# Kernel optimization log

Hardware: AMD Instinct MI355X
Metric: run time of the kernel (lower is better)

## Reference

```python
import jax, jax.numpy as jnp
import numpy as np
import math

B, N = 1, 768
C1, C2 = 384, 128
H, SQK, SV, PQK, PV, NC = 12, 16, 16, 4, 8, 384
EPS = 1e-8
SCALAR_W = math.sqrt(1.0 / (3.0 * SQK))           # sqrt(1/(num_logit_terms*scalar_variance))
POINT_W = math.sqrt(1.0 / (3.0 * (PQK * 9.0 / 2.0)))
W2D = math.sqrt(1.0 / 3.0)


def _quat_to_rot(q):
    # q: [..., 4] -> orthonormal rotation matrices [..., 3, 3]
    q = q / jnp.linalg.norm(q, axis=-1, keepdims=True)
    w, x, y, z = q[..., 0], q[..., 1], q[..., 2], q[..., 3]
    r0 = jnp.stack([1 - 2 * (y * y + z * z), 2 * (x * y - w * z), 2 * (x * z + w * y)], -1)
    r1 = jnp.stack([2 * (x * y + w * z), 1 - 2 * (x * x + z * z), 2 * (y * z - w * x)], -1)
    r2 = jnp.stack([2 * (x * z - w * y), 2 * (y * z + w * x), 1 - 2 * (x * x + y * y)], -1)
    return jnp.stack([r0, r1, r2], -2)


def setup_inputs() -> dict:
    key = jax.random.key(0)
    ks = jax.random.split(key, 12)

    def lin(k, o, i):
        kw, kb = jax.random.split(k)
        w = jax.random.normal(kw, (o, i), jnp.float32) / np.sqrt(i).astype(np.float32)
        b = jax.random.normal(kb, (o,), jnp.float32) * 0.01
        return w, b

    w_qs, b_qs = lin(ks[0], H * SQK, C1)
    w_kvs, b_kvs = lin(ks[1], H * (SV + SQK), C1)
    w_qp, b_qp = lin(ks[2], H * 3 * PQK, C1)
    w_kvp, b_kvp = lin(ks[3], H * 3 * (PQK + PV), C1)
    w_a2, b_a2 = lin(ks[4], H, C2)
    w_o, b_o = lin(ks[5], NC, H * (C2 + SV + 4 * PV))
    return {
        'inputs_1d': jax.random.normal(ks[6], (B, N, C1), jnp.float32),
        'inputs_2d': jax.random.normal(ks[7], (B, N, N, C2), jnp.float32),
        'mask': jnp.ones((B, N, 1), jnp.float32),
        'rotation': _quat_to_rot(jax.random.normal(ks[8], (B, N, 4), jnp.float32)),
        'translation': jax.random.normal(ks[9], (B, N, 3), jnp.float32) * 10.0,
        'w_q_scalar': w_qs, 'b_q_scalar': b_qs,
        'w_kv_scalar': w_kvs, 'b_kv_scalar': b_kvs,
        'w_q_point': w_qp, 'b_q_point': b_qp,
        'w_kv_point': w_kvp, 'b_kv_point': b_kvp,
        'tpw': jnp.ones((H,), jnp.float32),
        'w_attn2d': w_a2, 'b_attn2d': b_a2,
        'w_out': w_o, 'b_out': b_o,
    }


def ipa_forward(inputs_1d, inputs_2d, mask, rotation, translation,
                w_q_scalar, b_q_scalar, w_kv_scalar, b_kv_scalar,
                w_q_point, b_q_point, w_kv_point, b_kv_point,
                tpw, w_attn2d, b_attn2d, w_out, b_out):
    Bs, Ns, _ = inputs_1d.shape

    # scalar q/k/v
    q_scalar = (inputs_1d @ w_q_scalar.T + b_q_scalar).reshape(Bs, Ns, H, SQK)
    kv_scalar = (inputs_1d @ w_kv_scalar.T + b_kv_scalar).reshape(Bs, Ns, H, SQK + SV)
    k_scalar, v_scalar = kv_scalar[..., :SQK], kv_scalar[..., SQK:]

    # point q/k/v in local frame; split order is 3 coord chunks of size H*P
    qp = (inputs_1d @ w_q_point.T + b_q_point).reshape(Bs, Ns, 3, H * PQK)
    kvp = (inputs_1d @ w_kv_point.T + b_kv_point).reshape(Bs, Ns, 3, H * (PQK + PV))
    # to global frame: p_global = R @ p_local + t
    qg = jnp.einsum('bnij,bnjm->bnim', rotation, qp) + translation[..., None]
    kvg = jnp.einsum('bnij,bnjm->bnim', rotation, kvp) + translation[..., None]
    q_point = qg.reshape(Bs, Ns, 3, H, PQK).transpose(0, 3, 1, 4, 2)          # [B,H,N,Pqk,3]
    kv_point = kvg.reshape(Bs, Ns, 3, H, PQK + PV).transpose(0, 3, 1, 4, 2)    # [B,H,N,Pqk+Pv,3]
    k_point, v_point = kv_point[..., :PQK, :], kv_point[..., PQK:, :]

    # point-distance attention term: sum_{p,c} (q-k)^2 = |q|^2 + |k|^2 - 2 q.k
    pw = jax.nn.softplus(tpw) * POINT_W                                       # [H]
    qn = jnp.sum(q_point * q_point, axis=(-1, -2))                             # [B,H,N]
    kn = jnp.sum(k_point * k_point, axis=(-1, -2))
    qk = jnp.einsum('bhipc,bhjpc->bhij', q_point, k_point)
    dist2 = qn[..., :, None] + kn[..., None, :] - 2.0 * qk                     # [B,H,N,N]
    attn_qk_point = -0.5 * pw[None, :, None, None] * dist2

    # scalar attention term
    attn_qk_scalar = jnp.einsum('bihd,bjhd->bhij', SCALAR_W * q_scalar, k_scalar)

    # pair-bias term
    a2d = inputs_2d @ w_attn2d.T + b_attn2d                                    # [B,N,N,H]
    logits = attn_qk_scalar + attn_qk_point + W2D * a2d.transpose(0, 3, 1, 2)

    mask2d = mask * jnp.swapaxes(mask, -1, -2)                                 # [B,N,N]
    logits = logits - 1e5 * (1.0 - mask2d[:, None, :, :])
    attn = jax.nn.softmax(logits, axis=-1)                                     # [B,H,N,N]

    # scalar values
    result_scalar = jnp.einsum('bhij,bjhd->bihd', attn, v_scalar).reshape(Bs, Ns, H * SV)

    # point values (global), then back to local frame: p_local = R^T (p - t)
    rpg = jnp.einsum('bhij,bhjpc->bhipc', attn, v_point)                       # [B,H,N,Pv,3]
    rpg = rpg.transpose(0, 2, 4, 1, 3).reshape(Bs, Ns, 3, H * PV)              # [B,N,3,M]
    local = jnp.einsum('bnji,bnjm->bnim', rotation, rpg - translation[..., None])
    dist = jnp.sqrt(EPS + jnp.sum(local * local, axis=2))                      # [B,N,M]

    # attention over pair features
    r2d = jnp.einsum('bhij,bijc->bihc', attn, inputs_2d).reshape(Bs, Ns, H * C2)

    final_act = jnp.concatenate(
        [result_scalar, local[:, :, 0], local[:, :, 1], local[:, :, 2], dist, r2d], axis=-1)
    return final_act @ w_out.T + b_out


def reference(inputs_1d, inputs_2d, mask, rotation, translation,
              w_q_scalar, b_q_scalar, w_kv_scalar, b_kv_scalar,
              w_q_point, b_q_point, w_kv_point, b_kv_point,
              tpw, w_attn2d, b_attn2d, w_out, b_out):
    return ipa_forward(inputs_1d, inputs_2d, mask, rotation, translation,
                       w_q_scalar, b_q_scalar, w_kv_scalar, b_kv_scalar,
                       w_q_point, b_q_point, w_kv_point, b_kv_point,
                       tpw, w_attn2d, b_attn2d, w_out, b_out)
```

## Files before the change

### kernel.cpp

```cpp
#include <hip/hip_runtime.h>
#include <hip/hip_bf16.h>
#include <math.h>

#define NRES 768
#define C1 384
#define C2 128
#define NH 12
#define HB 6

#define OFF_QS   0
#define OFF_KS   147456
#define OFF_VS   294912
#define OFF_QPT  442368
#define OFF_KPT  552960
#define OFF_VPT  663552
#define OFF_FA   884736
#define OFF_RAW  OFF_FA

__device__ __forceinline__ float dot4(float4 a, float4 b) {
    return fmaf(a.x, b.x, fmaf(a.y, b.y, fmaf(a.z, b.z, a.w * b.w)));
}

static constexpr float SCALAR_W = 0.14433756729740643f;
static constexpr float POINT_W  = 0.13608276348795434f;
static constexpr float W2D_W    = 0.57735026918962576f;

__device__ __forceinline__ void wsel(int o,
    const float* w_qs, const float* b_qs, const float* w_kvs, const float* b_kvs,
    const float* w_qp, const float* b_qp, const float* w_kvp, const float* b_kvp,
    const float** row, float* bias)
{
    if (o < 192)      { *row = w_qs  + (size_t)o * C1;         *bias = b_qs[o]; }
    else if (o < 576) { *row = w_kvs + (size_t)(o - 192) * C1; *bias = b_kvs[o - 192]; }
    else if (o < 720) { *row = w_qp  + (size_t)(o - 576) * C1; *bias = b_qp[o - 576]; }
    else              { *row = w_kvp + (size_t)(o - 720) * C1; *bias = b_kvp[o - 720]; }
}

__global__ __launch_bounds__(256) void k1_gemm(
    const float* __restrict__ in1d,
    const float* __restrict__ w_qs, const float* __restrict__ b_qs,
    const float* __restrict__ w_kvs, const float* __restrict__ b_kvs,
    const float* __restrict__ w_qp, const float* __restrict__ b_qp,
    const float* __restrict__ w_kvp, const float* __restrict__ b_kvp,
    float* __restrict__ ws)
{
    __shared__ __align__(16) float ASt[32][68];
    __shared__ __align__(16) float WSt[32][68];
    const int t = threadIdx.x;
    const int n0 = blockIdx.x * 64;
    const int o0 = blockIdx.y * 64;
    const int tx = t & 15, ty = t >> 4;
    float acc[4][4];
    #pragma unroll
    for (int r = 0; r < 4; ++r)
        #pragma unroll
        for (int c = 0; c < 4; ++c) acc[r][c] = 0.f;

    for (int k0 = 0; k0 < C1; k0 += 32) {
        __syncthreads();
        #pragma unroll
        for (int s = 0; s < 2; ++s) {
            int q = t + 256 * s;
            int row = q >> 3, kq = (q & 7) * 4;
            float4 a4 = *(const float4*)&in1d[(size_t)(n0 + row) * C1 + k0 + kq];
            ASt[kq + 0][row] = a4.x; ASt[kq + 1][row] = a4.y;
            ASt[kq + 2][row] = a4.z; ASt[kq + 3][row] = a4.w;
            const float* wr; float bb;
            wsel(o0 + row, w_qs, b_qs, w_kvs, b_kvs, w_qp, b_qp, w_kvp, b_kvp, &wr, &bb);
            float4 w4 = *(const float4*)&wr[k0 + kq];
            WSt[kq + 0][row] = w4.x; WSt[kq + 1][row] = w4.y;
            WSt[kq + 2][row] = w4.z; WSt[kq + 3][row] = w4.w;
        }
        __syncthreads();
        #pragma unroll
        for (int k = 0; k < 32; ++k) {
            float4 a4 = *(const float4*)&ASt[k][ty * 4];
            float4 w4 = *(const float4*)&WSt[k][tx * 4];
            float av[4] = {a4.x, a4.y, a4.z, a4.w};
            float wv[4] = {w4.x, w4.y, w4.z, w4.w};
            #pragma unroll
            for (int r = 0; r < 4; ++r)
                #pragma unroll
                for (int c = 0; c < 4; ++c)
                    acc[r][c] = fmaf(av[r], wv[c], acc[r][c]);
        }
    }
    float bias[4];
    #pragma unroll
    for (int c = 0; c < 4; ++c) {
        const float* dummy;
        wsel(o0 + tx * 4 + c, w_qs, b_qs, w_kvs, b_kvs, w_qp, b_qp, w_kvp, b_kvp, &dummy, &bias[c]);
    }
    float* raw = ws + OFF_RAW;
    #pragma unroll
    for (int r = 0; r < 4; ++r) {
        int n = n0 + ty * 4 + r;
        *(float4*)&raw[(size_t)n * 1152 + o0 + tx * 4] =
            make_float4(acc[r][0] + bias[0], acc[r][1] + bias[1],
                        acc[r][2] + bias[2], acc[r][3] + bias[3]);
    }
}

__global__ __launch_bounds__(256) void k1b_scatter(
    const float* __restrict__ rot, const float* __restrict__ trans,
    float* __restrict__ ws)
{
    __shared__ __align__(16) float rawS[1152];
    const int t = threadIdx.x;
    const int i = blockIdx.x;
    const float* raw = ws + OFF_RAW + (size_t)i * 1152;
    for (int q = t; q < 288; q += 256) *(float4*)&rawS[q * 4] = *(const float4*)&raw[q * 4];
    __syncthreads();
    float* qs  = ws + OFF_QS;  float* ks  = ws + OFF_KS;  float* vs  = ws + OFF_VS;
    float* qpt = ws + OFF_QPT; float* kpt = ws + OFF_KPT; float* vpt = ws + OFF_VPT;

    for (int o = t; o < 576; o += 256) {
        float v = rawS[o];
        if (o < 192) {
            qs[(size_t)i * 192 + o] = v * SCALAR_W;
        } else {
            int idx = o - 192, h = idx >> 5, d = idx & 31;
            if (d < 16) ks[(size_t)i * 192 + h * 16 + d] = v;
            else        vs[(size_t)i * 192 + h * 16 + (d - 16)] = v;
        }
    }
    if (t < 192) {
        int m = t;
        float x0, x1, x2;
        if (m < 48) { x0 = rawS[576 + m]; x1 = rawS[624 + m]; x2 = rawS[672 + m]; }
        else { int mm = m - 48; x0 = rawS[720 + mm]; x1 = rawS[864 + mm]; x2 = rawS[1008 + mm]; }
        float g[3];
        #pragma unroll
        for (int ii = 0; ii < 3; ++ii)
            g[ii] = rot[i * 9 + ii * 3 + 0] * x0 + rot[i * 9 + ii * 3 + 1] * x1 +
                    rot[i * 9 + ii * 3 + 2] * x2 + trans[i * 3 + ii];
        if (m < 48) {
            #pragma unroll
            for (int ii = 0; ii < 3; ++ii) qpt[(size_t)i * 144 + 3 * m + ii] = g[ii];
        } else {
            int mm = m - 48, h = mm / 12, pp = mm % 12;
            if (pp < 4) {
                #pragma unroll
                for (int ii = 0; ii < 3; ++ii) kpt[(size_t)i * 144 + h * 12 + pp * 3 + ii] = g[ii];
            } else {
                #pragma unroll
                for (int ii = 0; ii < 3; ++ii) vpt[(size_t)i * 288 + h * 24 + (pp - 4) * 3 + ii] = g[ii];
            }
        }
    }
}

__global__ __launch_bounds__(256, 6) void k2_attn(
    const float* __restrict__ in2d,
    const float* __restrict__ mask,
    const float* __restrict__ rot, const float* __restrict__ trans,
    const float* __restrict__ tpw,
    const float* __restrict__ w2d, const float* __restrict__ b2d,
    float* __restrict__ ws)
{
    __shared__ __align__(16) float P[HB][264];
    __shared__ __align__(16) float qsS[192];
    __shared__ __align__(16) float qptS[144];
    __shared__ float qnS[HB], phS[HB], bbS[HB], mS[HB], lS[HB], aS[HB];
    __shared__ float rpgS[144];
    const int t  = threadIdx.x;
    const int hg = blockIdx.x;
    const int i  = blockIdx.y;
    const int h0 = hg * HB;

    const float* qs  = ws + OFF_QS;  const float* ks  = ws + OFF_KS;  const float* vs = ws + OFF_VS;
    const float* qpt = ws + OFF_QPT; const float* kpt = ws + OFF_KPT; const float* vpt = ws + OFF_VPT;

    if (t < 48) *(float4*)&qsS[t * 4] = *(const float4*)&qs[(size_t)i * 192 + t * 4];
    else if (t >= 64 && t < 100) { int u = t - 64; *(float4*)&qptS[u * 4] = *(const float4*)&qpt[(size_t)i * 144 + u * 4]; }
    __syncthreads();
    if (t < HB) {
        int h = h0 + t;
        float s = 0.f;
        #pragma unroll
        for (int e = 0; e < 12; ++e) { float x = qptS[h * 12 + e]; s += x * x; }
        qnS[t] = s;
        phS[t] = -0.5f * POINT_W * logf(1.f + __expf(tpw[h]));
        bbS[t] = W2D_W * b2d[h];
        mS[t] = -1e30f;
        lS[t] = 0.f;
    }
    __syncthreads();
    const float mi = mask[i];

    float ra[4] = {0.f, 0.f, 0.f, 0.f};
    float rb[4] = {0.f, 0.f, 0.f, 0.f};
    const bool isR2 = (t < 192);
    int lh = 0, c4 = 0, o0 = 0, q0 = 0, vh = 0;
    const float* vbase = nullptr; int vstride = 0; bool vact = false;
    if (isR2) { lh = t >> 5; c4 = t & 31; }
    else {
        int u = t - 192; vact = (u < 30); o0 = u * 8;
        if (vact) {
            if (u < 12) { vh = u >> 1; vbase = vs + (size_t)h0 * 16 + o0; vstride = 192; }
            else { q0 = o0 - 96; vh = q0 / 24; vbase = vpt + (size_t)h0 * 24 + q0; vstride = 288; }
        }
    }

    for (int tile = 0; tile < 3; ++tile) {
        const int j0 = tile * 256;
        __syncthreads();
        {
            const int j = j0 + t;
            float acc[HB];
            #pragma unroll
            for (int g = 0; g < HB; ++g) acc[g] = 0.f;
            const float* row   = in2d + ((size_t)i * NRES + j) * C2;
            const float* wbase = w2d + (size_t)h0 * C2;
            #pragma unroll 8
            for (int cc = 0; cc < 32; ++cc) {
                float4 v4 = *(const float4*)&row[cc * 4];
                #pragma unroll
                for (int g = 0; g < HB; ++g) {
                    float4 w4 = *(const float4*)&wbase[g * C2 + cc * 4];
                    acc[g] += dot4(v4, w4);
                }
            }
            const float msub = -100000.0f * (1.0f - mi * mask[j]);
            const float* ksr  = ks  + (size_t)j * 192 + h0 * 16;
            const float* kptr = kpt + (size_t)j * 144 + h0 * 12;
            #pragma unroll
            for (int g = 0; g < HB; ++g) {
                float sq = 0.f;
                #pragma unroll
                for (int d4 = 0; d4 < 4; ++d4) {
                    float4 q4 = *(const float4*)&qsS[(h0 + g) * 16 + d4 * 4];
                    float4 k4 = *(const float4*)&ksr[g * 16 + d4 * 4];
                    sq += dot4(q4, k4);
                }
                float qk = 0.f, kk = 0.f;
                #pragma unroll
                for (int e4 = 0; e4 < 3; ++e4) {
                    float4 qp4 = *(const float4*)&qptS[(h0 + g) * 12 + e4 * 4];
                    float4 kp4 = *(const float4*)&kptr[g * 12 + e4 * 4];
                    qk += dot4(qp4, kp4);
                    kk += dot4(kp4, kp4);
                }
                P[g][t] = sq + phS[g] * (qnS[g] + kk - 2.f * qk) + W2D_W * acc[g] + bbS[g] + msub;
            }
        }
        __syncthreads();
        {
            int wv = t >> 6, lane = t & 63;
            for (int g = wv; g < HB; g += 4) {
                float v0 = P[g][lane], v1 = P[g][lane + 64], v2 = P[g][lane + 128], v3 = P[g][lane + 192];
                float mt = fmaxf(fmaxf(v0, v1), fmaxf(v2, v3));
                #pragma unroll
                for (int off = 32; off > 0; off >>= 1) mt = fmaxf(mt, __shfl_xor(mt, off));
                float mold = mS[g];
                float mnew = fmaxf(mold, mt);
                float e0 = __expf(v0 - mnew), e1 = __expf(v1 - mnew);
                float e2 = __expf(v2 - mnew), e3 = __expf(v3 - mnew);
                P[g][lane] = e0; P[g][lane + 64] = e1; P[g][lane + 128] = e2; P[g][lane + 192] = e3;
                float s = e0 + e1 + e2 + e3;
                #pragma unroll
                for (int off = 32; off > 0; off >>= 1) s += __shfl_xor(s, off);
                if (lane == 0) {
                    float a = __expf(mold - mnew);
                    aS[g] = a;
                    lS[g] = lS[g] * a + s;
                    mS[g] = mnew;
                }
            }
        }
        __syncthreads();
        if (isR2) {
            float a = aS[lh];
            #pragma unroll
            for (int k = 0; k < 4; ++k) ra[k] *= a;
            const float* r2base = in2d + ((size_t)i * NRES + j0) * C2 + c4 * 4;
            for (int jj = 0; jj < 256; jj += 4) {
                float4 p4 = *(const float4*)&P[lh][jj];
                float w[4] = {p4.x, p4.y, p4.z, p4.w};
                #pragma unroll
                for (int k = 0; k < 4; ++k) {
                    float4 v4 = *(const float4*)&r2base[(size_t)(jj + k) * C2];
                    ra[0] = fmaf(w[k], v4.x, ra[0]); ra[1] = fmaf(w[k], v4.y, ra[1]);
                    ra[2] = fmaf(w[k], v4.z, ra[2]); ra[3] = fmaf(w[k], v4.w, ra[3]);
                }
            }
        } else if (vact) {
            float a = aS[vh];
            #pragma unroll
            for (int k = 0; k < 4; ++k) { ra[k] *= a; rb[k] *= a; }
            for (int jj = 0; jj < 256; jj += 4) {
                const int jg = j0 + jj;
                float4 p = *(const float4*)&P[vh][jj];
                float w[4] = {p.x, p.y, p.z, p.w};
                #pragma unroll
                for (int k = 0; k < 4; ++k) {
                    float4 va4 = *(const float4*)&vbase[(size_t)(jg + k) * vstride];
                    float4 vb4 = *(const float4*)&vbase[(size_t)(jg + k) * vstride + 4];
                    ra[0] = fmaf(w[k], va4.x, ra[0]); ra[1] = fmaf(w[k], va4.y, ra[1]);
                    ra[2] = fmaf(w[k], va4.z, ra[2]); ra[3] = fmaf(w[k], va4.w, ra[3]);
                    rb[0] = fmaf(w[k], vb4.x, rb[0]); rb[1] = fmaf(w[k], vb4.y, rb[1]);
                    rb[2] = fmaf(w[k], vb4.z, rb[2]); rb[3] = fmaf(w[k], vb4.w, rb[3]);
                }
            }
        }
    }
    float* fa = ws + OFF_FA + (size_t)i * 2112;
    if (isR2) {
        float nv = 1.f / lS[lh];
        *(float4*)&fa[576 + (h0 + lh) * 128 + c4 * 4] = make_float4(ra[0] * nv, ra[1] * nv, ra[2] * nv, ra[3] * nv);
    } else if (vact) {
        float nv = 1.f / lS[vh];
        if (o0 < 96) {
            *(float4*)&fa[h0 * 16 + o0]     = make_float4(ra[0] * nv, ra[1] * nv, ra[2] * nv, ra[3] * nv);
            *(float4*)&fa[h0 * 16 + o0 + 4] = make_float4(rb[0] * nv, rb[1] * nv, rb[2] * nv, rb[3] * nv);
        } else {
            *(float4*)&rpgS[q0]     = make_float4(ra[0] * nv, ra[1] * nv, ra[2] * nv, ra[3] * nv);
            *(float4*)&rpgS[q0 + 4] = make_float4(rb[0] * nv, rb[1] * nv, rb[2] * nv, rb[3] * nv);
        }
    }
    __syncthreads();
    if (t < 48) {
        int g = t >> 3, p = t & 7;
        int gh = h0 + g;
        float rv[3];
        #pragma unroll
        for (int c = 0; c < 3; ++c) rv[c] = rpgS[g * 24 + p * 3 + c] - trans[i * 3 + c];
        float l0 = rot[i * 9 + 0] * rv[0] + rot[i * 9 + 3] * rv[1] + rot[i * 9 + 6] * rv[2];
        float l1 = rot[i * 9 + 1] * rv[0] + rot[i * 9 + 4] * rv[1] + rot[i * 9 + 7] * rv[2];
        float l2 = rot[i * 9 + 2] * rv[0] + rot[i * 9 + 5] * rv[1] + rot[i * 9 + 8] * rv[2];
        float dd = sqrtf(1e-8f + l0 * l0 + l1 * l1 + l2 * l2);
        fa[192 + gh * 8 + p] = l0;
        fa[288 + gh * 8 + p] = l1;
        fa[384 + gh * 8 + p] = l2;
        fa[480 + gh * 8 + p] = dd;
    }
}

__global__ __launch_bounds__(256) void k3_out(
    const float* __restrict__ w_out, const float* __restrict__ b_out,
    const float* __restrict__ ws, float* __restrict__ out)
{
    __shared__ __align__(16) float ASt[32][34];
    __shared__ __align__(16) float WSt[32][34];
    const int t = threadIdx.x;
    const int i0 = blockIdx.x * 32;
    const int o0 = blockIdx.y * 32;
    const float* fa = ws + OFF_FA;
    int tx = t & 15, ty = t >> 4;
    float acc00 = 0.f, acc01 = 0.f, acc10 = 0.f, acc11 = 0.f;
    int r = t >> 3, kq = (t & 7) * 4;

    for (int k0 = 0; k0 < 2112; k0 += 32) {
        __syncthreads();
        {
            float4 a4 = *(const float4*)&fa[(size_t)(i0 + r) * 2112 + k0 + kq];
            ASt[kq + 0][r] = a4.x; ASt[kq + 1][r] = a4.y; ASt[kq + 2][r] = a4.z; ASt[kq + 3][r] = a4.w;
            float4 w4 = *(const float4*)&w_out[(size_t)(o0 + r) * 2112 + k0 + kq];
            WSt[kq + 0][r] = w4.x; WSt[kq + 1][r] = w4.y; WSt[kq + 2][r] = w4.z; WSt[kq + 3][r] = w4.w;
        }
        __syncthreads();
        #pragma unroll
        for (int k = 0; k < 32; ++k) {
            float2 av = *(const float2*)&ASt[k][ty * 2];
            float2 wv = *(const float2*)&WSt[k][tx * 2];
            acc00 = fmaf(av.x, wv.x, acc00);
            acc01 = fmaf(av.x, wv.y, acc01);
            acc10 = fmaf(av.y, wv.x, acc10);
            acc11 = fmaf(av.y, wv.y, acc11);
        }
    }
    int oi = i0 + ty * 2, oo = o0 + tx * 2;
    out[(size_t)oi * 384 + oo]           = acc00 + b_out[oo];
    out[(size_t)oi * 384 + oo + 1]       = acc01 + b_out[oo + 1];
    out[(size_t)(oi + 1) * 384 + oo]     = acc10 + b_out[oo];
    out[(size_t)(oi + 1) * 384 + oo + 1] = acc11 + b_out[oo + 1];
}

extern "C" void kernel_launch(void* const* d_in, const int* in_sizes, int n_in,
                              void* d_out, int out_size, void* d_ws, size_t ws_size,
                              hipStream_t stream) {
    const float* in1d  = (const float*)d_in[0];
    const float* in2d  = (const float*)d_in[1];
    const float* mask  = (const float*)d_in[2];
    const float* rot   = (const float*)d_in[3];
    const float* trans = (const float*)d_in[4];
    const float* w_qs  = (const float*)d_in[5];
    const float* b_qs  = (const float*)d_in[6];
    const float* w_kvs = (const float*)d_in[7];
    const float* b_kvs = (const float*)d_in[8];
    const float* w_qp  = (const float*)d_in[9];
    const float* b_qp  = (const float*)d_in[10];
    const float* w_kvp = (const float*)d_in[11];
    const float* b_kvp = (const float*)d_in[12];
    const float* tpw   = (const float*)d_in[13];
    const float* w2d   = (const float*)d_in[14];
    const float* b2d   = (const float*)d_in[15];
    const float* w_out = (const float*)d_in[16];
    const float* b_out = (const float*)d_in[17];
    float* ws  = (float*)d_ws;
    float* out = (float*)d_out;

    hipLaunchKernelGGL(k1_gemm, dim3(12, 18), dim3(256), 0, stream,
                       in1d, w_qs, b_qs, w_kvs, b_kvs, w_qp, b_qp, w_kvp, b_kvp, ws);
    hipLaunchKernelGGL(k1b_scatter, dim3(768), dim3(256), 0, stream,
                       rot, trans, ws);
    hipLaunchKernelGGL(k2_attn, dim3(2, 768), dim3(256), 0, stream,
                       in2d, mask, rot, trans, tpw, w2d, b2d, ws);
    hipLaunchKernelGGL(k3_out, dim3(24, 12), dim3(256), 0, stream,
                       w_out, b_out, ws, out);
}
```

Measured before the change: 871.1 us.

## Stage pair-feature tiles in shared memory and reorder attention grid

The pair-feature weighted sum now loads 32-row tiles of inputs_2d into shared memory cooperatively with all 256 threads, then the R2 threads read from LDS instead of doing strided global loads directly. The grid is also transposed so that consecutive blocks cover different residues i for the same head group. The tiling adds 16 syncthreads per chunk and 16 KB of LDS, which may lower occupancy under launch_bounds(256,6). It also still reads in2d once per head group.

New measurement: 882.4 us. Within noise of the previous version (+1.3%).

```diff
diff --git a/kernel.cpp b/kernel.cpp
--- a/kernel.cpp
+++ b/kernel.cpp
@@ -158,14 +158,15 @@
     const float* __restrict__ w2d, const float* __restrict__ b2d,
     float* __restrict__ ws)
 {
+    __shared__ __align__(16) float tileS[32][128];
     __shared__ __align__(16) float P[HB][264];
     __shared__ __align__(16) float qsS[192];
     __shared__ __align__(16) float qptS[144];
     __shared__ float qnS[HB], phS[HB], bbS[HB], mS[HB], lS[HB], aS[HB];
     __shared__ float rpgS[144];
     const int t  = threadIdx.x;
-    const int hg = blockIdx.x;
-    const int i  = blockIdx.y;
+    const int i  = blockIdx.x;
+    const int hg = blockIdx.y;
     const int h0 = hg * HB;
 
     const float* qs  = ws + OFF_QS;  const float* ks  = ws + OFF_KS;  const float* vs = ws + OFF_VS;
@@ -273,33 +274,48 @@
             float a = aS[lh];
             #pragma unroll
             for (int k = 0; k < 4; ++k) ra[k] *= a;
-            const float* r2base = in2d + ((size_t)i * NRES + j0) * C2 + c4 * 4;
-            for (int jj = 0; jj < 256; jj += 4) {
-                float4 p4 = *(const float4*)&P[lh][jj];
-                float w[4] = {p4.x, p4.y, p4.z, p4.w};
-                #pragma unroll
-                for (int k = 0; k < 4; ++k) {
-                    float4 v4 = *(const float4*)&r2base[(size_t)(jj + k) * C2];
-                    ra[0] = fmaf(w[k], v4.x, ra[0]); ra[1] = fmaf(w[k], v4.y, ra[1]);
-                    ra[2] = fmaf(w[k], v4.z, ra[2]); ra[3] = fmaf(w[k], v4.w, ra[3]);
-                }
-            }
         } else if (vact) {
             float a = aS[vh];
             #pragma unroll
             for (int k = 0; k < 4; ++k) { ra[k] *= a; rb[k] *= a; }
-            for (int jj = 0; jj < 256; jj += 4) {
-                const int jg = j0 + jj;
-                float4 p = *(const float4*)&P[vh][jj];
-                float w[4] = {p.x, p.y, p.z, p.w};
-                #pragma unroll
-                for (int k = 0; k < 4; ++k) {
-                    float4 va4 = *(const float4*)&vbase[(size_t)(jg + k) * vstride];
-                    float4 vb4 = *(const float4*)&vbase[(size_t)(jg + k) * vstride + 4];
-                    ra[0] = fmaf(w[k], va4.x, ra[0]); ra[1] = fmaf(w[k], va4.y, ra[1]);
-                    ra[2] = fmaf(w[k], va4.z, ra[2]); ra[3] = fmaf(w[k], va4.w, ra[3]);
-                    rb[0] = fmaf(w[k], vb4.x, rb[0]); rb[1] = fmaf(w[k], vb4.y, rb[1]);
-                    rb[2] = fmaf(w[k], vb4.z, rb[2]); rb[3] = fmaf(w[k], vb4.w, rb[3]);
+        }
+        for (int sub = 0; sub < 8; ++sub) {
+            __syncthreads();
+            #pragma unroll
+            for (int u2 = 0; u2 < 4; ++u2) {
+                int q = u2 * 256 + t;
+                int rr = q >> 5, cc = q & 31;
+                *(float4*)&tileS[rr][cc * 4] =
+                    *(const float4*)&in2d[((size_t)i * NRES + j0 + sub * 32 + rr) * C2 + cc * 4];
+            }
+            __syncthreads();
+            if (isR2) {
+                for (int jj = 0; jj < 32; jj += 4) {
+                    int jt = sub * 32 + jj;
+                    float4 p4 = *(const float4*)&P[lh][jt];
+                    float w[4] = {p4.x, p4.y, p4.z, p4.w};
+                    #pragma unroll
+                    for (int k = 0; k < 4; ++k) {
+                        float4 v4 = *(const float4*)&tileS[jj + k][c4 * 4];
+                        ra[0] = fmaf(w[k], v4.x, ra[0]); ra[1] = fmaf(w[k], v4.y, ra[1]);
+                        ra[2] = fmaf(w[k], v4.z, ra[2]); ra[3] = fmaf(w[k], v4.w, ra[3]);
+                    }
+                }
+            } else if (vact) {
+                for (int jj = 0; jj < 32; jj += 4) {
+                    int jt = sub * 32 + jj;
+                    int jg = j0 + jt;
+                    float4 p = *(const float4*)&P[vh][jt];
+                    float w[4] = {p.x, p.y, p.z, p.w};
+                    #pragma unroll
+                    for (int k = 0; k < 4; ++k) {
+                        float4 va4 = *(const float4*)&vbase[(size_t)(jg + k) * vstride];
+                        float4 vb4 = *(const float4*)&vbase[(size_t)(jg + k) * vstride + 4];
+                        ra[0] = fmaf(w[k], va4.x, ra[0]); ra[1] = fmaf(w[k], va4.y, ra[1]);
+                        ra[2] = fmaf(w[k], va4.z, ra[2]); ra[3] = fmaf(w[k], va4.w, ra[3]);
+                        rb[0] = fmaf(w[k], vb4.x, rb[0]); rb[1] = fmaf(w[k], vb4.y, rb[1]);
+                        rb[2] = fmaf(w[k], vb4.z, rb[2]); rb[3] = fmaf(w[k], vb4.w, rb[3]);
+                    }
                 }
             }
         }
@@ -404,7 +420,7 @@
                        in1d, w_qs, b_qs, w_kvs, b_kvs, w_qp, b_qp, w_kvp, b_kvp, ws);
     hipLaunchKernelGGL(k1b_scatter, dim3(768), dim3(256), 0, stream,
                        rot, trans, ws);
-    hipLaunchKernelGGL(k2_attn, dim3(2, 768), dim3(256), 0, stream,
+    hipLaunchKernelGGL(k2_attn, dim3(768, 2), dim3(256), 0, stream,
                        in2d, mask, rot, trans, tpw, w2d, b2d, ws);
     hipLaunchKernelGGL(k3_out, dim3(24, 12), dim3(256), 0, stream,
                        w_out, b_out, ws, out);
```
